# Optimization experiments

Measured on AMD Instinct MI355X. Metric: run time of the kernel, lower is better.

Reference implementation:

```python
import jax, jax.numpy as jnp
import numpy as np

DEPTH = 6
H = 12
D = 768
FF = 4 * D
OUT_INDICES = (2, 5)
EPS = 1e-5


def layernorm(x, g, b):
    m = jnp.mean(x, axis=-1, keepdims=True)
    v = jnp.mean(jnp.square(x - m), axis=-1, keepdims=True)
    return (x - m) * jax.lax.rsqrt(v + EPS) * g + b


def setup_inputs() -> dict:
    key = jax.random.key(0)
    ks = jax.random.split(key, 8)
    B, N = 2, 1024
    s = 0.02
    inp = {
        "x": jax.random.normal(ks[0], (B, N, D), dtype=jnp.float32),
        "rel_bias": jax.random.normal(ks[1], (H, N, N), dtype=jnp.float32),
        "ln1_g": jnp.ones((DEPTH, D), jnp.float32),
        "ln1_b": jnp.zeros((DEPTH, D), jnp.float32),
        "qkv_w": jax.random.normal(ks[2], (DEPTH, D, 3 * D), dtype=jnp.float32) * s,
        "out_w": jax.random.normal(ks[3], (DEPTH, D, D), dtype=jnp.float32) * s,
        "out_b": jnp.zeros((DEPTH, D), jnp.float32),
        "ln2_g": jnp.ones((DEPTH, D), jnp.float32),
        "ln2_b": jnp.zeros((DEPTH, D), jnp.float32),
        "ff1_w": jax.random.normal(ks[4], (DEPTH, D, FF), dtype=jnp.float32) * s,
        "ff1_b": jnp.zeros((DEPTH, FF), jnp.float32),
        "ff2_w": jax.random.normal(ks[5], (DEPTH, FF, D), dtype=jnp.float32) * s,
        "ff2_b": jnp.zeros((DEPTH, D), jnp.float32),
        "lnf_g": jnp.ones((D,), jnp.float32),
        "lnf_b": jnp.zeros((D,), jnp.float32),
    }
    return inp


def reference(x, rel_bias, ln1_g, ln1_b, qkv_w, out_w, out_b, ln2_g, ln2_b,
              ff1_w, ff1_b, ff2_w, ff2_b, lnf_g, lnf_b):
    B, N, Dm = x.shape
    Dh = Dm // H
    scale = Dh ** -0.5
    kside = int(round(N ** 0.5))  # N is a perfect square (patch grid)
    feats = []
    for i in range(DEPTH):
        # --- attention block ---
        h = layernorm(x, ln1_g[i], ln1_b[i])
        qkv = h @ qkv_w[i]                                   # [B,N,3D]
        q, k, v = jnp.split(qkv, 3, axis=-1)
        q = q.reshape(B, N, H, Dh).transpose(0, 2, 1, 3)     # [B,H,N,Dh]
        k = k.reshape(B, N, H, Dh).transpose(0, 2, 1, 3)
        v = v.reshape(B, N, H, Dh).transpose(0, 2, 1, 3)
        scores = jnp.einsum('bhid,bhjd->bhij', q, k) * scale + rel_bias
        attn = jax.nn.softmax(scores, axis=-1)
        o = jnp.einsum('bhij,bhjd->bhid', attn, v)
        o = o.transpose(0, 2, 1, 3).reshape(B, N, Dm)
        x = x + (o @ out_w[i] + out_b[i])
        # --- FFN block ---
        h2 = layernorm(x, ln2_g[i], ln2_b[i])
        ff = jax.nn.gelu(h2 @ ff1_w[i] + ff1_b[i], approximate=False)
        x = x + (ff @ ff2_w[i] + ff2_b[i])
        if i in OUT_INDICES:
            feats.append(x.reshape(B, kside, kside, Dm).transpose(0, 3, 1, 2))
    xf = layernorm(x, lnf_g, lnf_b)
    return (xf, *feats)
```

## Files before the change

### kernel.cpp

```cpp
#include <hip/hip_runtime.h>
#include <hip/hip_bf16.h>

typedef unsigned short ushort_t;
typedef __attribute__((ext_vector_type(8))) __bf16 bf16x8;
typedef __attribute__((ext_vector_type(8))) unsigned short u16x8;
typedef __attribute__((ext_vector_type(4))) float f32x4;
typedef __attribute__((ext_vector_type(4))) unsigned int u32x4;

#define DEPTH 6
#define HEADS 12
#define DMODEL 768
#define FFDIM 3072
#define BATCH 2
#define SEQ 1024
#define ROWS (BATCH * SEQ)

static __device__ __forceinline__ ushort_t f2bf(float f) {
  unsigned u = __builtin_bit_cast(unsigned, f);
  u += 0x7fffu + ((u >> 16) & 1u);
  return (ushort_t)(u >> 16);
}
static __device__ __forceinline__ float bf2f(ushort_t v) {
  return __builtin_bit_cast(float, (unsigned)v << 16);
}

template <int MREP, int NREP, int EPI>
__global__ __launch_bounds__(256) void gemm_bt(
    const ushort_t* __restrict__ A, const ushort_t* __restrict__ Bt,
    int lda, int ldb, int K,
    void* __restrict__ out0, void* __restrict__ out1,
    const float* __restrict__ f0) {
  constexpr int BM = 32 * MREP;
  constexpr int BN = 32 * NREP;
  constexpr int CHA = BM / 32;
  constexpr int CHB = BN / 32;
  __shared__ ushort_t sA[2][BM * 64];
  __shared__ ushort_t sB[2][BN * 64];

  const int tid = threadIdx.x;
  const int lane = tid & 63;
  const int wid = tid >> 6;
  const int wm = wid >> 1, wn = wid & 1;

  int bx, by;
  {
    const int nb = gridDim.x * gridDim.y;
    const int bid = blockIdx.y * gridDim.x + blockIdx.x;
    const int q = nb >> 3;
    const int swz = (bid & 7) * q + (bid >> 3);
    bx = swz % gridDim.x;
    by = swz / gridDim.x;
  }

  const ushort_t* Ab = A + (long)bx * BM * lda;
  const ushort_t* Bb = Bt + (long)by * BN * ldb;

  const int srow = lane >> 3;
  const int scol = ((lane & 7) ^ srow) * 8;

  f32x4 acc[MREP][NREP];
#pragma unroll
  for (int m = 0; m < MREP; ++m)
#pragma unroll
    for (int n = 0; n < NREP; ++n) acc[m][n] = (f32x4){0.f, 0.f, 0.f, 0.f};

  const int fr = lane & 15;
  const int kq4 = lane >> 4;

  auto stage_tile = [&](int buf, int t) {
    const int k0 = t * 64;
#pragma unroll
    for (int j = 0; j < CHA; ++j) {
      const int c = wid * CHA + j;
      const ushort_t* src = Ab + (long)(c * 8 + srow) * lda + k0 + scol;
      __builtin_amdgcn_global_load_lds(
          (const __attribute__((address_space(1))) void*)src,
          (__attribute__((address_space(3))) void*)&sA[buf][c * 512], 16, 0, 0);
    }
#pragma unroll
    for (int j = 0; j < CHB; ++j) {
      const int c = wid * CHB + j;
      const ushort_t* src = Bb + (long)(c * 8 + srow) * ldb + k0 + scol;
      __builtin_amdgcn_global_load_lds(
          (const __attribute__((address_space(1))) void*)src,
          (__attribute__((address_space(3))) void*)&sB[buf][c * 512], 16, 0, 0);
    }
  };

  const int nt = K / 64;
  stage_tile(0, 0);
  for (int t = 0; t < nt; ++t) {
    const int cur = t & 1;
    asm volatile("s_waitcnt vmcnt(0)" ::: "memory");
    __builtin_amdgcn_s_barrier();
    if (t + 1 < nt) stage_tile(cur ^ 1, t + 1);
#pragma unroll
    for (int kk = 0; kk < 2; ++kk) {
      bf16x8 af[MREP], bfr[NREP];
#pragma unroll
      for (int m = 0; m < MREP; ++m) {
        const int row = wm * (MREP * 16) + m * 16 + fr;
        const int ch = (kk * 4 + kq4) ^ (row & 7);
        af[m] = *(const bf16x8*)&sA[cur][row * 64 + ch * 8];
      }
#pragma unroll
      for (int n = 0; n < NREP; ++n) {
        const int row = wn * (NREP * 16) + n * 16 + fr;
        const int ch = (kk * 4 + kq4) ^ (row & 7);
        bfr[n] = *(const bf16x8*)&sB[cur][row * 64 + ch * 8];
      }
#pragma unroll
      for (int m = 0; m < MREP; ++m)
#pragma unroll
        for (int n = 0; n < NREP; ++n)
          acc[m][n] = __builtin_amdgcn_mfma_f32_16x16x32_bf16(
              af[m], bfr[n], acc[m][n], 0, 0, 0);
    }
  }

  const long grow0 = (long)bx * BM + wm * (MREP * 16);
  const long gcol0 = (long)by * BN + wn * (NREP * 16);
  const int rr = (lane >> 4) * 4;
  const int cc = lane & 15;

#pragma unroll
  for (int m = 0; m < MREP; ++m) {
#pragma unroll
    for (int n = 0; n < NREP; ++n) {
#pragma unroll
      for (int r = 0; r < 4; ++r) {
        long row = grow0 + m * 16 + rr + r;
        long col = gcol0 + n * 16 + cc;
        float c = acc[m][n][r];
        if (EPI == 0) {
          ushort_t bv = f2bf(c);
          if (col < 1536) {
            ((ushort_t*)out0)[row * 2304 + col] = bv;
          } else {
            long h = (col - 1536) >> 6, d = (col - 1536) & 63;
            long b = row >> 10, i = row & 1023;
            ((ushort_t*)out1)[(((b * HEADS) + h) * 64 + d) * 1024 + i] = bv;
          }
        } else if (EPI == 3) {
          long idx = row * DMODEL + col;
          ((float*)out0)[idx] += c + f0[col];
        } else if (EPI == 4) {
          float t = c + f0[col];
          float g = 0.5f * t * (1.0f + erff(t * 0.70710678118f));
          ((ushort_t*)out0)[row * FFDIM + col] = f2bf(g);
        } else if (EPI == 5) {
          long idx = row * DMODEL + col;
          ((float*)out0)[idx] += c + f0[col];
        }
      }
    }
  }
}

__global__ __launch_bounds__(256) void pack_bias(const float* __restrict__ rel,
                                                 ushort_t* __restrict__ pb) {
  __shared__ ushort_t tile[1024];
  const int blk = blockIdx.x;
  const int t = blk & 15, qi = (blk >> 4) & 63, h = blk >> 10;
  const float* src = rel + ((size_t)h << 20) + (size_t)(qi * 16) * 1024 + t * 64;
  const int tid = threadIdx.x;
  const int kk = tid & 63;
#pragma unroll
  for (int it = 0; it < 4; ++it) {
    const int qr = (tid >> 6) * 4 + it;
    const float v = src[(size_t)qr * 1024 + kk];
    const int lane = (qr >> 2) * 16 + (kk & 15);
    const int idx = (kk >> 4) * 4 + (qr & 3);
    tile[lane * 16 + idx] = f2bf(v);
  }
  __syncthreads();
  ushort_t* dst = pb + (size_t)blk * 1024;
#pragma unroll
  for (int it = 0; it < 4; ++it) dst[it * 256 + tid] = tile[it * 256 + tid];
}

__global__ __launch_bounds__(128) void flash_attn(
    const ushort_t* __restrict__ qkv,
    const ushort_t* __restrict__ vt,
    const ushort_t* __restrict__ pbias,
    ushort_t* __restrict__ o) {
  __shared__ ushort_t sK[2][64 * 64];
  __shared__ ushort_t sV[2][64 * 64];
  __shared__ ushort_t sP[32 * 64];

  const int tid = threadIdx.x;
  const int lane = tid & 63;
  const int wid = tid >> 6;
  const int h = blockIdx.y, b = blockIdx.z;
  const int q0 = blockIdx.x * 32;
  const int qi = blockIdx.x * 2 + wid;

  const int fr = lane & 15;
  const int kq4 = lane >> 4;
  const int rr = kq4 * 4;
  const int cc = fr;

  const int srow = lane >> 3;
  const int scol = ((lane & 7) ^ srow) * 8;

  const ushort_t* qbase =
      qkv + (size_t)(b * 1024 + q0 + wid * 16 + fr) * 2304 + h * 64;
  bf16x8 qreg[2];
  qreg[0] = *(const bf16x8*)&qbase[kq4 * 8];
  qreg[1] = *(const bf16x8*)&qbase[32 + kq4 * 8];

  const ushort_t* Kbase = qkv + (size_t)(b * 1024) * 2304 + 768 + h * 64;
  const ushort_t* Vbase = vt + (size_t)((b * HEADS + h) * 64) * 1024;
  const ushort_t* pbb = pbias + (((size_t)h * 64 + qi) << 14) + lane * 16;

  f32x4 acc_o[4];
  float m_run[4], l_run[4];
#pragma unroll
  for (int n = 0; n < 4; ++n) acc_o[n] = (f32x4){0.f, 0.f, 0.f, 0.f};
#pragma unroll
  for (int r = 0; r < 4; ++r) { m_run[r] = -1e30f; l_run[r] = 0.f; }

  auto stage_kv = [&](int buf, int t) {
#pragma unroll
    for (int j = 0; j < 4; ++j) {
      const int c = wid * 4 + j;
      const ushort_t* src = Kbase + (size_t)(t * 64 + c * 8 + srow) * 2304 + scol;
      __builtin_amdgcn_global_load_lds(
          (const __attribute__((address_space(1))) void*)src,
          (__attribute__((address_space(3))) void*)&sK[buf][c * 512], 16, 0, 0);
    }
#pragma unroll
    for (int j = 0; j < 4; ++j) {
      const int c = wid * 4 + j;
      const ushort_t* src = Vbase + (size_t)(c * 8 + srow) * 1024 + t * 64 + scol;
      __builtin_amdgcn_global_load_lds(
          (const __attribute__((address_space(1))) void*)src,
          (__attribute__((address_space(3))) void*)&sV[buf][c * 512], 16, 0, 0);
    }
  };

  auto step = [&](int t, u16x8& bc0, u16x8& bc1, u16x8& bn0, u16x8& bn1) {
    const int cur = t & 1;
    asm volatile("s_waitcnt vmcnt(0)" ::: "memory");
    __builtin_amdgcn_s_barrier();
    if (t + 1 < 16) {
      stage_kv(cur ^ 1, t + 1);
      const ushort_t* pp = pbb + (size_t)(t + 1) * 1024;
      bn0 = *(const u16x8*)pp;
      bn1 = *(const u16x8*)(pp + 8);
    }

    f32x4 s[4];
#pragma unroll
    for (int n = 0; n < 4; ++n) s[n] = (f32x4){0.f, 0.f, 0.f, 0.f};
    __builtin_amdgcn_s_setprio(1);
#pragma unroll
    for (int kk = 0; kk < 2; ++kk) {
#pragma unroll
      for (int n = 0; n < 4; ++n) {
        const int row = n * 16 + fr;
        const int ch = (kk * 4 + kq4) ^ (row & 7);
        bf16x8 kf = *(const bf16x8*)&sK[cur][row * 64 + ch * 8];
        s[n] =
            __builtin_amdgcn_mfma_f32_16x16x32_bf16(qreg[kk], kf, s[n], 0, 0, 0);
      }
    }
    __builtin_amdgcn_s_setprio(0);

    float mr[4];
#pragma unroll
    for (int r = 0; r < 4; ++r) mr[r] = -1e30f;
#pragma unroll
    for (int n = 0; n < 4; ++n)
#pragma unroll
      for (int r = 0; r < 4; ++r) {
        const int idx = n * 4 + r;
        const float bv = bf2f(idx < 8 ? bc0[idx] : bc1[idx - 8]);
        float v = s[n][r] * 0.125f + bv;
        s[n][r] = v;
        mr[r] = fmaxf(mr[r], v);
      }
#pragma unroll
    for (int o_ = 1; o_ < 16; o_ <<= 1)
#pragma unroll
      for (int r = 0; r < 4; ++r) mr[r] = fmaxf(mr[r], __shfl_xor(mr[r], o_));

    float escale[4], psum[4];
#pragma unroll
    for (int r = 0; r < 4; ++r) {
      float mn = fmaxf(m_run[r], mr[r]);
      escale[r] = __expf(m_run[r] - mn);
      m_run[r] = mn;
      psum[r] = 0.f;
    }
#pragma unroll
    for (int n = 0; n < 4; ++n)
#pragma unroll
      for (int r = 0; r < 4; ++r) {
        float p = __expf(s[n][r] - m_run[r]);
        psum[r] += p;
        const int prow = wid * 16 + rr + r;
        const int pcol = n * 16 + cc;
        sP[prow * 64 + (((pcol >> 3) ^ (prow & 7)) << 3) + (pcol & 7)] = f2bf(p);
      }
#pragma unroll
    for (int o_ = 1; o_ < 16; o_ <<= 1)
#pragma unroll
      for (int r = 0; r < 4; ++r) psum[r] += __shfl_xor(psum[r], o_);
#pragma unroll
    for (int r = 0; r < 4; ++r) l_run[r] = l_run[r] * escale[r] + psum[r];


#pragma unroll
    for (int n = 0; n < 4; ++n)
#pragma unroll
      for (int r = 0; r < 4; ++r) acc_o[n][r] *= escale[r];
    __builtin_amdgcn_s_setprio(1);
#pragma unroll
    for (int kk = 0; kk < 2; ++kk) {
      const int prow = wid * 16 + fr;
      const int pch = (kk * 4 + kq4) ^ (prow & 7);
      bf16x8 pf = *(const bf16x8*)&sP[prow * 64 + pch * 8];
#pragma unroll
      for (int n = 0; n < 4; ++n) {
        const int vrow = n * 16 + fr;
        const int vch = (kk * 4 + kq4) ^ (vrow & 7);
        bf16x8 vf = *(const bf16x8*)&sV[cur][vrow * 64 + vch * 8];
        acc_o[n] =
            __builtin_amdgcn_mfma_f32_16x16x32_bf16(pf, vf, acc_o[n], 0, 0, 0);
      }
    }
    __builtin_amdgcn_s_setprio(0);
  };

  u16x8 bA0, bA1, bB0, bB1;
  bA0 = *(const u16x8*)pbb;
  bA1 = *(const u16x8*)(pbb + 8);
  stage_kv(0, 0);
  for (int tt = 0; tt < 16; tt += 2) {
    step(tt, bA0, bA1, bB0, bB1);
    step(tt + 1, bB0, bB1, bA0, bA1);
  }

  ushort_t* ob = o + (size_t)(b * 1024 + q0 + wid * 16) * 768 + h * 64;
#pragma unroll
  for (int r = 0; r < 4; ++r) {
    const float rinv = 1.f / l_run[r];
#pragma unroll
    for (int n = 0; n < 4; ++n)
      ob[(size_t)(rr + r) * 768 + n * 16 + cc] = f2bf(acc_o[n][r] * rinv);
  }
}

__global__ __launch_bounds__(256) void transpose_cast(
    const float* __restrict__ in, ushort_t* __restrict__ out, int R, int C) {
  __shared__ float t[32][33];
  const float* ip = in + (long)blockIdx.z * R * C;
  ushort_t* op = out + (long)blockIdx.z * R * C;
  int c0 = blockIdx.x * 32, r0 = blockIdx.y * 32;
  int tx = threadIdx.x;
  for (int i = threadIdx.y; i < 32; i += 8)
    t[i][tx] = ip[(long)(r0 + i) * C + c0 + tx];
  __syncthreads();
  for (int i = threadIdx.y; i < 32; i += 8)
    op[(long)(c0 + i) * R + r0 + tx] = f2bf(t[tx][i]);
}

__global__ __launch_bounds__(256) void ln_kernel(
    const float* __restrict__ x, const float* __restrict__ g,
    const float* __restrict__ b, void* __restrict__ out, int out_f32) {
  int row = blockIdx.x;
  int tid = threadIdx.x;
  int lane = tid & 63, wid = tid >> 6;
  const float* xr = x + (long)row * DMODEL;
  float v0 = xr[tid], v1 = xr[tid + 256], v2 = xr[tid + 512];
  float s = v0 + v1 + v2;
  __shared__ float red[8];
  for (int o = 32; o; o >>= 1) s += __shfl_xor(s, o);
  if (!lane) red[wid] = s;
  __syncthreads();
  float mean = (red[0] + red[1] + red[2] + red[3]) * (1.f / 768.f);
  float d0 = v0 - mean, d1 = v1 - mean, d2 = v2 - mean;
  float q = d0 * d0 + d1 * d1 + d2 * d2;
  for (int o = 32; o; o >>= 1) q += __shfl_xor(q, o);
  if (!lane) red[4 + wid] = q;
  __syncthreads();
  float var = (red[4] + red[5] + red[6] + red[7]) * (1.f / 768.f);
  float rs = rsqrtf(var + 1e-5f);
  float y0 = d0 * rs * g[tid] + b[tid];
  float y1 = d1 * rs * g[tid + 256] + b[tid + 256];
  float y2 = d2 * rs * g[tid + 512] + b[tid + 512];
  if (out_f32) {
    float* o_ = (float*)out + (long)row * DMODEL;
    o_[tid] = y0; o_[tid + 256] = y1; o_[tid + 512] = y2;
  } else {
    ushort_t* o_ = (ushort_t*)out + (long)row * DMODEL;
    o_[tid] = f2bf(y0); o_[tid + 256] = f2bf(y1); o_[tid + 512] = f2bf(y2);
  }
}

__global__ __launch_bounds__(256) void feat_kernel(const float* __restrict__ x,
                                                   float* __restrict__ out) {
  __shared__ float t[32][33];
  const float* xp = x + (long)blockIdx.z * SEQ * DMODEL;
  float* op = out + (long)blockIdx.z * DMODEL * SEQ;
  int n0 = blockIdx.x * 32, c0 = blockIdx.y * 32;
  int tx = threadIdx.x;
  for (int i = threadIdx.y; i < 32; i += 8)
    t[i][tx] = xp[(long)(n0 + i) * DMODEL + c0 + tx];
  __syncthreads();
  for (int i = threadIdx.y; i < 32; i += 8)
    op[(long)(c0 + i) * SEQ + n0 + tx] = t[tx][i];
}

extern "C" void kernel_launch(void* const* d_in, const int* in_sizes, int n_in,
                              void* d_out, int out_size, void* d_ws,
                              size_t ws_size, hipStream_t stream) {
  const float* x_in   = (const float*)d_in[0];
  const float* rel    = (const float*)d_in[1];
  const float* ln1_g  = (const float*)d_in[2];
  const float* ln1_b  = (const float*)d_in[3];
  const float* qkv_w  = (const float*)d_in[4];
  const float* out_w  = (const float*)d_in[5];
  const float* out_b  = (const float*)d_in[6];
  const float* ln2_g  = (const float*)d_in[7];
  const float* ln2_b  = (const float*)d_in[8];
  const float* ff1_w  = (const float*)d_in[9];
  const float* ff1_b  = (const float*)d_in[10];
  const float* ff2_w  = (const float*)d_in[11];
  const float* ff2_b  = (const float*)d_in[12];
  const float* lnf_g  = (const float*)d_in[13];
  const float* lnf_b  = (const float*)d_in[14];
  float* out = (float*)d_out;

  char* w = (char*)d_ws;
  ushort_t* wq_t = (ushort_t*)w; w += (size_t)DEPTH * 2304 * 768 * 2;
  ushort_t* wo_t = (ushort_t*)w; w += (size_t)DEPTH * 768 * 768 * 2;
  ushort_t* wf1_t = (ushort_t*)w; w += (size_t)DEPTH * 3072 * 768 * 2;
  ushort_t* wf2_t = (ushort_t*)w; w += (size_t)DEPTH * 768 * 3072 * 2;
  float* xb = (float*)w; w += (size_t)ROWS * DMODEL * 4;
  ushort_t* hb = (ushort_t*)w; w += (size_t)ROWS * DMODEL * 2;
  ushort_t* qkvb = (ushort_t*)w; w += (size_t)ROWS * 2304 * 2;
  ushort_t* vt = (ushort_t*)w; w += (size_t)BATCH * HEADS * 64 * 1024 * 2;
  ushort_t* ob = (ushort_t*)w; w += (size_t)ROWS * DMODEL * 2;
  ushort_t* ffb = (ushort_t*)w; w += (size_t)ROWS * FFDIM * 2;
  ushort_t* pbias = (ushort_t*)w; w += (size_t)HEADS * 1024 * 1024 * 2;

  dim3 tb(32, 8);
  transpose_cast<<<dim3(2304 / 32, 768 / 32, DEPTH), tb, 0, stream>>>(
      qkv_w, wq_t, 768, 2304);
  transpose_cast<<<dim3(768 / 32, 768 / 32, DEPTH), tb, 0, stream>>>(
      out_w, wo_t, 768, 768);
  transpose_cast<<<dim3(3072 / 32, 768 / 32, DEPTH), tb, 0, stream>>>(
      ff1_w, wf1_t, 768, 3072);
  transpose_cast<<<dim3(768 / 32, 3072 / 32, DEPTH), tb, 0, stream>>>(
      ff2_w, wf2_t, 3072, 768);
  pack_bias<<<HEADS * 64 * 16, 256, 0, stream>>>(rel, pbias);

  hipMemcpyAsync(xb, x_in, (size_t)ROWS * DMODEL * 4, hipMemcpyDeviceToDevice,
                 stream);

  for (int i = 0; i < DEPTH; ++i) {
    ln_kernel<<<ROWS, 256, 0, stream>>>(xb, ln1_g + i * 768, ln1_b + i * 768,
                                        hb, 0);
    gemm_bt<2, 2, 0><<<dim3(32, 36), 256, 0, stream>>>(
        hb, wq_t + (size_t)i * 2304 * 768, 768, 768, 768, qkvb, vt, nullptr);
    flash_attn<<<dim3(32, HEADS, BATCH), 128, 0, stream>>>(qkvb, vt, pbias, ob);
    gemm_bt<1, 2, 3><<<dim3(64, 12), 256, 0, stream>>>(
        ob, wo_t + (size_t)i * 768 * 768, 768, 768, 768, xb, nullptr,
        out_b + i * 768);
    ln_kernel<<<ROWS, 256, 0, stream>>>(xb, ln2_g + i * 768, ln2_b + i * 768,
                                        hb, 0);
    gemm_bt<2, 2, 4><<<dim3(32, 48), 256, 0, stream>>>(
        hb, wf1_t + (size_t)i * 3072 * 768, 768, 768, 768, ffb, nullptr,
        ff1_b + i * 3072);
    gemm_bt<1, 2, 5><<<dim3(64, 12), 256, 0, stream>>>(
        ffb, wf2_t + (size_t)i * 768 * 3072, 3072, 3072, 3072, xb, nullptr,
        ff2_b + i * 768);
    if (i == 2)
      feat_kernel<<<dim3(32, 24, 2), tb, 0, stream>>>(xb, out + 1572864);
    if (i == 5)
      feat_kernel<<<dim3(32, 24, 2), tb, 0, stream>>>(xb, out + 2 * 1572864);
  }
  ln_kernel<<<ROWS, 256, 0, stream>>>(xb, lnf_g, lnf_b, out, 1);
}
```

Measured before the change: 933.4 us.

## Software-pipeline QK^T of next tile with softmax and PV of current tile

Restructures the flash-attention inner loop so each iteration issues the QK^T MFMAs for tile i while the softmax and PV for tile i-1 are still pending. This lets matrix-core work overlap with the exp, reduction and shuffle work inside a wave. V moves to a triple buffer, since its tile is now read one iteration after staging, while K stays double-buffered. The loop is fully unrolled, and two score accumulators are kept, which raises register pressure and code size and may cost occupancy.

```diff
diff --git a/kernel.cpp b/kernel.cpp
--- a/kernel.cpp
+++ b/kernel.cpp
@@ -185,7 +185,7 @@
     const ushort_t* __restrict__ pbias,
     ushort_t* __restrict__ o) {
   __shared__ ushort_t sK[2][64 * 64];
-  __shared__ ushort_t sV[2][64 * 64];
+  __shared__ ushort_t sV[3][64 * 64];
   __shared__ ushort_t sP[32 * 64];
 
   const int tid = threadIdx.x;
@@ -220,14 +220,14 @@
 #pragma unroll
   for (int r = 0; r < 4; ++r) { m_run[r] = -1e30f; l_run[r] = 0.f; }
 
-  auto stage_kv = [&](int buf, int t) {
+  auto stage_kv = [&](int kbuf, int vbuf, int t) {
 #pragma unroll
     for (int j = 0; j < 4; ++j) {
       const int c = wid * 4 + j;
       const ushort_t* src = Kbase + (size_t)(t * 64 + c * 8 + srow) * 2304 + scol;
       __builtin_amdgcn_global_load_lds(
           (const __attribute__((address_space(1))) void*)src,
-          (__attribute__((address_space(3))) void*)&sK[buf][c * 512], 16, 0, 0);
+          (__attribute__((address_space(3))) void*)&sK[kbuf][c * 512], 16, 0, 0);
     }
 #pragma unroll
     for (int j = 0; j < 4; ++j) {
@@ -235,22 +235,11 @@
       const ushort_t* src = Vbase + (size_t)(c * 8 + srow) * 1024 + t * 64 + scol;
       __builtin_amdgcn_global_load_lds(
           (const __attribute__((address_space(1))) void*)src,
-          (__attribute__((address_space(3))) void*)&sV[buf][c * 512], 16, 0, 0);
+          (__attribute__((address_space(3))) void*)&sV[vbuf][c * 512], 16, 0, 0);
     }
   };
 
-  auto step = [&](int t, u16x8& bc0, u16x8& bc1, u16x8& bn0, u16x8& bn1) {
-    const int cur = t & 1;
-    asm volatile("s_waitcnt vmcnt(0)" ::: "memory");
-    __builtin_amdgcn_s_barrier();
-    if (t + 1 < 16) {
-      stage_kv(cur ^ 1, t + 1);
-      const ushort_t* pp = pbb + (size_t)(t + 1) * 1024;
-      bn0 = *(const u16x8*)pp;
-      bn1 = *(const u16x8*)(pp + 8);
-    }
-
-    f32x4 s[4];
+  auto qk = [&](f32x4* s, int kbuf) {
 #pragma unroll
     for (int n = 0; n < 4; ++n) s[n] = (f32x4){0.f, 0.f, 0.f, 0.f};
     __builtin_amdgcn_s_setprio(1);
@@ -260,13 +249,15 @@
       for (int n = 0; n < 4; ++n) {
         const int row = n * 16 + fr;
         const int ch = (kk * 4 + kq4) ^ (row & 7);
-        bf16x8 kf = *(const bf16x8*)&sK[cur][row * 64 + ch * 8];
+        bf16x8 kf = *(const bf16x8*)&sK[kbuf][row * 64 + ch * 8];
         s[n] =
             __builtin_amdgcn_mfma_f32_16x16x32_bf16(qreg[kk], kf, s[n], 0, 0, 0);
       }
     }
     __builtin_amdgcn_s_setprio(0);
-
+  };
+
+  auto soft_pv = [&](f32x4* s, const u16x8& b0, const u16x8& b1, int vbuf) {
     float mr[4];
 #pragma unroll
     for (int r = 0; r < 4; ++r) mr[r] = -1e30f;
@@ -275,7 +266,7 @@
 #pragma unroll
       for (int r = 0; r < 4; ++r) {
         const int idx = n * 4 + r;
-        const float bv = bf2f(idx < 8 ? bc0[idx] : bc1[idx - 8]);
+        const float bv = bf2f(idx < 8 ? b0[idx] : b1[idx - 8]);
         float v = s[n][r] * 0.125f + bv;
         s[n][r] = v;
         mr[r] = fmaxf(mr[r], v);
@@ -310,7 +301,6 @@
 #pragma unroll
     for (int r = 0; r < 4; ++r) l_run[r] = l_run[r] * escale[r] + psum[r];
 
-
 #pragma unroll
     for (int n = 0; n < 4; ++n)
 #pragma unroll
@@ -325,7 +315,7 @@
       for (int n = 0; n < 4; ++n) {
         const int vrow = n * 16 + fr;
         const int vch = (kk * 4 + kq4) ^ (vrow & 7);
-        bf16x8 vf = *(const bf16x8*)&sV[cur][vrow * 64 + vch * 8];
+        bf16x8 vf = *(const bf16x8*)&sV[vbuf][vrow * 64 + vch * 8];
         acc_o[n] =
             __builtin_amdgcn_mfma_f32_16x16x32_bf16(pf, vf, acc_o[n], 0, 0, 0);
       }
@@ -334,12 +324,36 @@
   };
 
   u16x8 bA0, bA1, bB0, bB1;
+  f32x4 sE[4], sO[4];
+
+  stage_kv(0, 0, 0);
+  asm volatile("s_waitcnt vmcnt(0)" ::: "memory");
+  __builtin_amdgcn_s_barrier();
+  stage_kv(1, 1, 1);
   bA0 = *(const u16x8*)pbb;
   bA1 = *(const u16x8*)(pbb + 8);
-  stage_kv(0, 0);
-  for (int tt = 0; tt < 16; tt += 2) {
-    step(tt, bA0, bA1, bB0, bB1);
-    step(tt + 1, bB0, bB1, bA0, bA1);
+  qk(sE, 0);
+
+#pragma unroll
+  for (int i = 1; i <= 16; ++i) {
+    if (i < 16) {
+      asm volatile("s_waitcnt vmcnt(0)" ::: "memory");
+      __builtin_amdgcn_s_barrier();
+      if (i < 15) stage_kv((i + 1) & 1, (i + 1) % 3, i + 1);
+      const ushort_t* pp = pbb + (size_t)i * 1024;
+      if (i & 1) {
+        bB0 = *(const u16x8*)pp;
+        bB1 = *(const u16x8*)(pp + 8);
+        qk(sO, i & 1);
+      } else {
+        bA0 = *(const u16x8*)pp;
+        bA1 = *(const u16x8*)(pp + 8);
+        qk(sE, i & 1);
+      }
+    }
+    const int j = i - 1;
+    if (j & 1) soft_pv(sO, bB0, bB1, j % 3);
+    else soft_pv(sE, bA0, bA1, j % 3);
   }
 
   ushort_t* ob = o + (size_t)(b * 1024 + q0 + wid * 16) * 768 + h * 64;
```

Result: no change. 939.3 us (+0.6%).
